# Kernel tuning notes

Measured on AMD Instinct MI355X. Metric: run time of the kernel, lower is better.

Reference implementation:

```python
import jax, jax.numpy as jnp
import numpy as np

N_HEADS = 16
THRESHOLD = 0.01
GROWTH_RATE = 0.05
NEG_INF = -1e30


def setup_inputs() -> dict:
    key = jax.random.key(0)
    k1, k2, k3, k4, k5 = jax.random.split(key, 5)
    B, T, C = 2, 2048, 1024
    s_in = 1.0 / np.sqrt(C)
    return {
        "x": jax.random.normal(k1, (B, T, C), dtype=jnp.float32),
        "Wqkv": jax.random.normal(k2, (C, 3 * C), dtype=jnp.float32) * s_in,
        "bqkv": jnp.zeros((3 * C,), dtype=jnp.float32),
        "Wout": jax.random.normal(k3, (C, C), dtype=jnp.float32) * s_in,
        "bout": jnp.zeros((C,), dtype=jnp.float32),
    }


def reference(x, Wqkv, bqkv, Wout, bout):
    B, T, C = x.shape
    H = N_HEADS
    D = C // H
    scale = jnp.float32(np.sqrt(D))

    qkv = x @ Wqkv + bqkv                         # [B,T,3C]
    qkv = qkv.reshape(B, T, 3, H, D)
    q = qkv[:, :, 0].transpose(0, 2, 1, 3)        # [B,H,T,D]
    k = qkv[:, :, 1].transpose(0, 2, 1, 3)
    v = qkv[:, :, 2].transpose(0, 2, 1, 3)

    scores = jnp.einsum('bhtd,bhsd->bhts', q, k) / scale   # [B,H,T,T]
    causal = jnp.tril(jnp.ones((T, T), dtype=bool))
    scores = jnp.where(causal, scores, NEG_INF)
    attn = jax.nn.softmax(scores, axis=-1)

    # neuroplastic sparsification: threshold prune + random regrow
    # (training-mode path; fixed key for determinism, dropout treated as identity/eval)
    regrow = jax.random.uniform(jax.random.key(42), attn.shape) < GROWTH_RATE
    keep = jnp.logical_or(attn > THRESHOLD, regrow)
    attn = attn * keep.astype(attn.dtype)

    out = jnp.einsum('bhts,bhsd->bhtd', attn, v)  # [B,H,T,D]
    out = out.transpose(0, 2, 1, 3).reshape(B, T, C)
    return out @ Wout + bout
```

## Files before the change

kernel.cpp:

```cpp
#include <hip/hip_runtime.h>
#include <stdint.h>


typedef _Float16 half8 __attribute__((ext_vector_type(8)));
typedef _Float16 half4 __attribute__((ext_vector_type(4)));
typedef float f32x4 __attribute__((ext_vector_type(4)));

#define MFMA16(a, b, c) __builtin_amdgcn_mfma_f32_16x16x32_f16(a, b, c, 0, 0, 0)

__device__ __forceinline__ void gld16(const void* g, void* l) {
  __builtin_amdgcn_global_load_lds(
      (const __attribute__((address_space(1))) void*)g,
      (__attribute__((address_space(3))) void*)l, 16, 0, 0);
}

__device__ __forceinline__ uint32_t rotl32(uint32_t x, uint32_t d) {
  return (x << d) | (x >> (32u - d));
}

__device__ __forceinline__ bool regrow(uint32_t b, uint32_t hts) {
  const uint32_t ks1 = 42u;
  const uint32_t ks2 = 0x1BD11BDAu ^ 42u;
  uint32_t x0 = 0u;
  uint32_t x1 = b * 0x4000000u + hts;
  x1 += ks1;
#define TF_R(r) { x0 += x1; x1 = rotl32(x1, r); x1 ^= x0; }
  TF_R(13) TF_R(15) TF_R(26) TF_R(6)  x0 += ks1; x1 += ks2 + 1u;
  TF_R(17) TF_R(29) TF_R(16) TF_R(24) x0 += ks2; x1 += 0u  + 2u;
  TF_R(13) TF_R(15) TF_R(26) TF_R(6)  x0 += 0u;  x1 += ks1 + 3u;
  TF_R(17) TF_R(29) TF_R(16) TF_R(24) x0 += ks1; x1 += ks2 + 4u;
  TF_R(13) TF_R(15) TF_R(26) TF_R(6)  x0 += ks2; x1 += 0u  + 5u;
#undef TF_R
  uint32_t r32 = x0 ^ x1;
  float f = __uint_as_float((r32 >> 9) | 0x3f800000u) - 1.0f;
  return f < 0.05f;
}

__global__ __launch_bounds__(256) void conv_x(const float* __restrict__ x,
                                              _Float16* __restrict__ xh,
                                              _Float16* __restrict__ xl) {
  int idx = blockIdx.x * 256 + threadIdx.x;
  int row = idx >> 7;
  int c8 = (idx & 127) << 3;
  const float* s = x + (size_t)row * 1024 + c8;
  float4 v0 = *(const float4*)s;
  float4 v1 = *(const float4*)(s + 4);
  float vv[8] = {v0.x, v0.y, v0.z, v0.w, v1.x, v1.y, v1.z, v1.w};
  half8 hh, ll;
#pragma unroll
  for (int i = 0; i < 8; ++i) {
    hh[i] = (_Float16)vv[i];
    ll[i] = (_Float16)(vv[i] - (float)hh[i]);
  }
  size_t o = (size_t)row * 1024 + (c8 ^ ((row & 7) << 3));
  *(half8*)&xh[o] = hh;
  *(half8*)&xl[o] = ll;
}

__global__ __launch_bounds__(256) void conv_w(const float* __restrict__ W, int N,
                                              _Float16* __restrict__ Wth,
                                              _Float16* __restrict__ Wtl) {
  __shared__ float sW[64][68];
  const int n0 = blockIdx.x * 64, k0 = blockIdx.y * 64;
  const int t = threadIdx.x;
  const int kr = t >> 2, nc = (t & 3) * 16;
#pragma unroll
  for (int j = 0; j < 4; ++j)
    *(float4*)&sW[kr][nc + 4 * j] =
        *(const float4*)&W[(size_t)(k0 + kr) * N + n0 + nc + 4 * j];
  __syncthreads();
  const int nl = t >> 2, ks = (t & 3) * 16;
#pragma unroll
  for (int j = 0; j < 2; ++j) {
    int k8 = ks + j * 8;
    half8 hh, ll;
#pragma unroll
    for (int e = 0; e < 8; ++e) {
      float v = sW[k8 + e][nl];
      hh[e] = (_Float16)v;
      ll[e] = (_Float16)(v - (float)hh[e]);
    }
    size_t o = (size_t)(n0 + nl) * 1024 + ((k0 + k8) ^ (((n0 + nl) & 7) << 3));
    *(half8*)&Wth[o] = hh;
    *(half8*)&Wtl[o] = ll;
  }
}

template <int PRE>
__global__ __launch_bounds__(256) void gemm_f16x3(
    const _Float16* __restrict__ Ah, const _Float16* __restrict__ Al,
    const float* __restrict__ Afp,
    const _Float16* __restrict__ Bth, const _Float16* __restrict__ Btl,
    const float* __restrict__ bias, int N, int outMode,
    _Float16* __restrict__ Qh, _Float16* __restrict__ Ql,
    _Float16* __restrict__ Kh, _Float16* __restrict__ Kl,
    _Float16* __restrict__ Vt, float* __restrict__ out)
{
  __shared__ _Float16 sAh[8192], sAl[8192], sBh[8192], sBl[8192];
  const int tid = threadIdx.x;
  const int wv = tid >> 6, lane = tid & 63;
  const int lg = lane >> 4, m15 = lane & 15;
  const int wr = wv >> 1, wc = wv & 1;
  const int m0 = blockIdx.y << 7, n0 = blockIdx.x << 7;
  const int srow = lane >> 3;
  const int schk = (lane & 7) << 3;

  f32x4 acc[4][4];
#pragma unroll
  for (int i = 0; i < 4; ++i)
#pragma unroll
    for (int j = 0; j < 4; ++j) acc[i][j] = (f32x4){0.f, 0.f, 0.f, 0.f};

  for (int g = 0; g < 16; ++g) {
    __syncthreads();
#pragma unroll
    for (int i = 0; i < 4; ++i) {
      int rb = (wv << 5) + (i << 3);
      size_t so = (size_t)(n0 + rb + srow) * 1024 + (g << 6) + schk;
      gld16(Bth + so, &sBh[rb << 6]);
      gld16(Btl + so, &sBl[rb << 6]);
    }
    if (PRE) {
#pragma unroll
      for (int i = 0; i < 4; ++i) {
        int rb = (wv << 5) + (i << 3);
        size_t so = (size_t)(m0 + rb + srow) * 1024 + (g << 6) + schk;
        gld16(Ah + so, &sAh[rb << 6]);
        gld16(Al + so, &sAl[rb << 6]);
      }
    } else {
      int r = tid >> 1, c0 = (tid & 1) << 5;
      const float* src = Afp + (size_t)(m0 + r) * 1024 + (g << 6) + c0;
#pragma unroll
      for (int i = 0; i < 8; ++i) {
        float4 v = *(const float4*)(src + (i << 2));
        half4 hh = {(_Float16)v.x, (_Float16)v.y, (_Float16)v.z, (_Float16)v.w};
        half4 ll = {(_Float16)(v.x - (float)hh[0]), (_Float16)(v.y - (float)hh[1]),
                    (_Float16)(v.z - (float)hh[2]), (_Float16)(v.w - (float)hh[3])};
        int off = (r << 6) + ((c0 + (i << 2)) ^ ((r & 7) << 3));
        *(half4*)&sAh[off] = hh;
        *(half4*)&sAl[off] = ll;
      }
    }
    __syncthreads();

#pragma unroll
    for (int ks = 0; ks < 2; ++ks) {
      half8 ah[4], al[4], bh[4], bl[4];
#pragma unroll
      for (int mi = 0; mi < 4; ++mi) {
        int row = (wr << 6) + (mi << 4) + m15;
        int off = (row << 6) + (((ks << 5) + (lg << 3)) ^ ((row & 7) << 3));
        ah[mi] = *(const half8*)&sAh[off];
        al[mi] = *(const half8*)&sAl[off];
      }
#pragma unroll
      for (int nj = 0; nj < 4; ++nj) {
        int row = (wc << 6) + (nj << 4) + m15;
        int off = (row << 6) + (((ks << 5) + (lg << 3)) ^ ((row & 7) << 3));
        bh[nj] = *(const half8*)&sBh[off];
        bl[nj] = *(const half8*)&sBl[off];
      }
#pragma unroll
      for (int mi = 0; mi < 4; ++mi)
#pragma unroll
        for (int nj = 0; nj < 4; ++nj) {
          acc[mi][nj] = MFMA16(ah[mi], bh[nj], acc[mi][nj]);
          acc[mi][nj] = MFMA16(ah[mi], bl[nj], acc[mi][nj]);
          acc[mi][nj] = MFMA16(al[mi], bh[nj], acc[mi][nj]);
        }
    }
  }

#pragma unroll
  for (int nj = 0; nj < 4; ++nj) {
    int n = n0 + (wc << 6) + (nj << 4) + m15;
    float bv = bias[n];
    int which = n >> 10;
    int hh_ = (n & 1023) >> 6;
    int d = n & 63;
#pragma unroll
    for (int mi = 0; mi < 4; ++mi) {
#pragma unroll
      for (int r = 0; r < 4; ++r) {
        int m = m0 + (wr << 6) + (mi << 4) + (lg << 2) + r;
        float v = acc[mi][nj][r] + bv;
        if (outMode == 1) {
          out[(size_t)m * N + n] = v;
        } else {
          _Float16 hi = (_Float16)v;
          _Float16 lo = (_Float16)(v - (float)hi);
          int b = m >> 11, t = m & 2047;
          if (which == 2) {
            size_t o = ((size_t)((b << 4) + hh_) * 64 + d) * 2048
                     + (t ^ ((d & 7) << 3));
            Vt[o] = hi;
          } else {
            size_t o = ((size_t)((b << 4) + hh_) * 2048 + t) * 64
                     + (d ^ ((t & 7) << 3));
            if (which == 0) { Qh[o] = hi; Ql[o] = lo; }
            else            { Kh[o] = hi; Kl[o] = lo; }
          }
        }
      }
    }
  }
}

__global__ __launch_bounds__(256) void attn_mfma(
    const _Float16* __restrict__ Qhg, const _Float16* __restrict__ Qlg,
    const _Float16* __restrict__ Khg, const _Float16* __restrict__ Klg,
    const _Float16* __restrict__ Vtg,
    _Float16* __restrict__ AOh, _Float16* __restrict__ AOl)
{
  __shared__ _Float16 sQh[4096], sQl[4096], sKh[4096], sKl[4096];
  __shared__ _Float16 sVt[4096], sP[4096];

  const int tid = threadIdx.x;
  const int wv = tid >> 6, lane = tid & 63;
  const int lg = lane >> 4, m15 = lane & 15;
  const int h = blockIdx.y, b = blockIdx.z;
  const size_t bh = (size_t)(b * 16 + h);
  const _Float16* Qhb = Qhg + bh * 2048 * 64;
  const _Float16* Qlb = Qlg + bh * 2048 * 64;
  const _Float16* Khb = Khg + bh * 2048 * 64;
  const _Float16* Klb = Klg + bh * 2048 * 64;
  const _Float16* Vtb = Vtg + bh * 64 * 2048;

  const int srow = lane >> 3, schk = (lane & 7) << 3;
  const int w16 = wv << 4;

  for (int hv = 0; hv < 2; ++hv) {
    const int qt = hv ? (31 - (int)blockIdx.x) : (int)blockIdx.x;
    const int t0 = qt << 6;

    __syncthreads();
    {
      size_t o0 = (size_t)(t0 + w16 + srow) * 64 + schk;
      size_t o1 = (size_t)(t0 + w16 + 8 + srow) * 64 + schk;
      gld16(Qhb + o0, &sQh[w16 << 6]);
      gld16(Qhb + o1, &sQh[(w16 + 8) << 6]);
      gld16(Qlb + o0, &sQl[w16 << 6]);
      gld16(Qlb + o1, &sQl[(w16 + 8) << 6]);
    }
    __syncthreads();

    const int qrow = w16 + m15;
    const int qsw = (qrow & 7) << 3;
    const half8 qh0 = *(const half8*)&sQh[(qrow << 6) + ((lg << 3) ^ qsw)];
    const half8 qh1 = *(const half8*)&sQh[(qrow << 6) + (((lg << 3) + 32) ^ qsw)];
    const half8 ql0 = *(const half8*)&sQl[(qrow << 6) + ((lg << 3) ^ qsw)];
    const half8 ql1 = *(const half8*)&sQl[(qrow << 6) + (((lg << 3) + 32) ^ qsw)];

    float m_[4], l_[4];
#pragma unroll
    for (int r = 0; r < 4; ++r) { m_[r] = -INFINITY; l_[r] = 0.0f; }

    for (int kt = 0; kt <= qt; ++kt) {
      __syncthreads();
      {
        size_t o0 = (size_t)((kt << 6) + w16 + srow) * 64 + schk;
        size_t o1 = (size_t)((kt << 6) + w16 + 8 + srow) * 64 + schk;
        gld16(Khb + o0, &sKh[w16 << 6]);
        gld16(Khb + o1, &sKh[(w16 + 8) << 6]);
        gld16(Klb + o0, &sKl[w16 << 6]);
        gld16(Klb + o1, &sKl[(w16 + 8) << 6]);
      }
      __syncthreads();

      float sc[4][4];
#pragma unroll
      for (int nt = 0; nt < 4; ++nt) {
        const int krow = (nt << 4) + m15;
        const int ksw = (krow & 7) << 3;
        half8 kh0 = *(const half8*)&sKh[(krow << 6) + ((lg << 3) ^ ksw)];
        half8 kh1 = *(const half8*)&sKh[(krow << 6) + (((lg << 3) + 32) ^ ksw)];
        half8 kl0 = *(const half8*)&sKl[(krow << 6) + ((lg << 3) ^ ksw)];
        half8 kl1 = *(const half8*)&sKl[(krow << 6) + (((lg << 3) + 32) ^ ksw)];
        f32x4 c = {0.f, 0.f, 0.f, 0.f};
        c = MFMA16(qh0, kh0, c);
        c = MFMA16(qh1, kh1, c);
        c = MFMA16(qh0, kl0, c);
        c = MFMA16(qh1, kl1, c);
        c = MFMA16(ql0, kh0, c);
        c = MFMA16(ql1, kh1, c);
#pragma unroll
        for (int r = 0; r < 4; ++r) {
          float s = c[r] * 0.125f;
          if (kt == qt && ((nt << 4) + m15) > (w16 + (lg << 2) + r)) s = -1e30f;
          sc[nt][r] = s;
        }
      }
#pragma unroll
      for (int r = 0; r < 4; ++r) {
        float tm = fmaxf(fmaxf(sc[0][r], sc[1][r]), fmaxf(sc[2][r], sc[3][r]));
        tm = fmaxf(tm, __shfl_xor(tm, 1));
        tm = fmaxf(tm, __shfl_xor(tm, 2));
        tm = fmaxf(tm, __shfl_xor(tm, 4));
        tm = fmaxf(tm, __shfl_xor(tm, 8));
        float mn = fmaxf(m_[r], tm);
        float ps = __expf(sc[0][r] - mn) + __expf(sc[1][r] - mn)
                 + __expf(sc[2][r] - mn) + __expf(sc[3][r] - mn);
        ps += __shfl_xor(ps, 1);
        ps += __shfl_xor(ps, 2);
        ps += __shfl_xor(ps, 4);
        ps += __shfl_xor(ps, 8);
        l_[r] = l_[r] * __expf(m_[r] - mn) + ps;
        m_[r] = mn;
      }
    }

    float rl[4];
#pragma unroll
    for (int r = 0; r < 4; ++r) rl[r] = 1.0f / l_[r];

    f32x4 oacc[4];
#pragma unroll
    for (int nt = 0; nt < 4; ++nt) oacc[nt] = (f32x4){0.f, 0.f, 0.f, 0.f};

    const uint32_t hqbase = (uint32_t)(h * 2048 + t0 + w16 + (lg << 2)) * 2048u;

    for (int kt = 0; kt <= qt; ++kt) {
      __syncthreads();
      {
        size_t o0 = (size_t)((kt << 6) + w16 + srow) * 64 + schk;
        size_t o1 = (size_t)((kt << 6) + w16 + 8 + srow) * 64 + schk;
        gld16(Khb + o0, &sKh[w16 << 6]);
        gld16(Khb + o1, &sKh[(w16 + 8) << 6]);
        gld16(Klb + o0, &sKl[w16 << 6]);
        gld16(Klb + o1, &sKl[(w16 + 8) << 6]);
        size_t v0 = (size_t)(w16 + srow) * 2048 + (kt << 6) + schk;
        size_t v1 = (size_t)(w16 + 8 + srow) * 2048 + (kt << 6) + schk;
        gld16(Vtb + v0, &sVt[w16 << 6]);
        gld16(Vtb + v1, &sVt[(w16 + 8) << 6]);
      }
      __syncthreads();

      float sc[4][4];
#pragma unroll
      for (int nt = 0; nt < 4; ++nt) {
        const int krow = (nt << 4) + m15;
        const int ksw = (krow & 7) << 3;
        half8 kh0 = *(const half8*)&sKh[(krow << 6) + ((lg << 3) ^ ksw)];
        half8 kh1 = *(const half8*)&sKh[(krow << 6) + (((lg << 3) + 32) ^ ksw)];
        half8 kl0 = *(const half8*)&sKl[(krow << 6) + ((lg << 3) ^ ksw)];
        half8 kl1 = *(const half8*)&sKl[(krow << 6) + (((lg << 3) + 32) ^ ksw)];
        f32x4 c = {0.f, 0.f, 0.f, 0.f};
        c = MFMA16(qh0, kh0, c);
        c = MFMA16(qh1, kh1, c);
        c = MFMA16(qh0, kl0, c);
        c = MFMA16(qh1, kl1, c);
        c = MFMA16(ql0, kh0, c);
        c = MFMA16(ql1, kh1, c);
#pragma unroll
        for (int r = 0; r < 4; ++r) {
          float s = c[r] * 0.125f;
          if (kt == qt && ((nt << 4) + m15) > (w16 + (lg << 2) + r)) s = -1e30f;
          sc[nt][r] = s;
        }
      }

#pragma unroll
      for (int nt = 0; nt < 4; ++nt) {
#pragma unroll
        for (int r = 0; r < 4; ++r) {
          float pv = __expf(sc[nt][r] - m_[r]) * rl[r];
          float outp = 0.0f;
          if (pv > 0.01f) {
            outp = pv;
          } else if (pv > 0.0f) {
            uint32_t hts = hqbase + (uint32_t)r * 2048u
                         + (uint32_t)((kt << 6) + (nt << 4) + m15);
            if (regrow((uint32_t)b, hts)) outp = pv;
          }
          int q = w16 + (lg << 2) + r;
          sP[(q << 6) + (((nt << 4) + m15) ^ ((q & 7) << 3))] = (_Float16)outp;
        }
      }
      __syncthreads();

      const int prow = w16 + m15;
      const int psw = (prow & 7) << 3;
      half8 pa0 = *(const half8*)&sP[(prow << 6) + ((lg << 3) ^ psw)];
      half8 pa1 = *(const half8*)&sP[(prow << 6) + (((lg << 3) + 32) ^ psw)];
#pragma unroll
      for (int nt = 0; nt < 4; ++nt) {
        const int vrow = (nt << 4) + m15;
        const int vsw = (vrow & 7) << 3;
        half8 vb0 = *(const half8*)&sVt[(vrow << 6) + ((lg << 3) ^ vsw)];
        half8 vb1 = *(const half8*)&sVt[(vrow << 6) + (((lg << 3) + 32) ^ vsw)];
        oacc[nt] = MFMA16(pa0, vb0, oacc[nt]);
        oacc[nt] = MFMA16(pa1, vb1, oacc[nt]);
      }
    }

#pragma unroll
    for (int nt = 0; nt < 4; ++nt)
#pragma unroll
      for (int r = 0; r < 4; ++r) {
        int q = t0 + w16 + (lg << 2) + r;
        int col = (h << 6) + (nt << 4) + m15;
        int mrow = (b << 11) + q;
        float v = oacc[nt][r];
        _Float16 hi = (_Float16)v;
        _Float16 lo = (_Float16)(v - (float)hi);
        size_t o = (size_t)mrow * 1024 + (col ^ ((mrow & 7) << 3));
        AOh[o] = hi;
        AOl[o] = lo;
      }
  }
}

extern "C" void kernel_launch(void* const* d_in, const int* in_sizes, int n_in,
                              void* d_out, int out_size, void* d_ws, size_t ws_size,
                              hipStream_t stream) {
  const float* x    = (const float*)d_in[0];
  const float* Wqkv = (const float*)d_in[1];
  const float* bqkv = (const float*)d_in[2];
  const float* Wout = (const float*)d_in[3];
  const float* bout = (const float*)d_in[4];
  float* out = (float*)d_out;

  const size_t MB = 1u << 20;
  char* w = (char*)d_ws;
  _Float16* Qh = (_Float16*)(w);
  _Float16* Ql = (_Float16*)(w + 8 * MB);
  _Float16* Kh = (_Float16*)(w + 16 * MB);
  _Float16* Kl = (_Float16*)(w + 24 * MB);
  _Float16* Vt = (_Float16*)(w + 32 * MB);

  const bool pre = (ws_size >= 72 * MB);
  _Float16 *xh, *xl, *Wqh, *Wql, *Woh, *Wol, *AOh, *AOl;
  if (pre) {
    xh  = (_Float16*)(w + 40 * MB);
    xl  = (_Float16*)(w + 48 * MB);
    Wqh = (_Float16*)(w + 56 * MB);
    Wql = (_Float16*)(w + 62 * MB);
    Woh = (_Float16*)(w + 68 * MB);
    Wol = (_Float16*)(w + 70 * MB);
  } else {
    xh = xl = nullptr;
    Wqh = (_Float16*)(w + 40 * MB);
    Wql = (_Float16*)(w + 46 * MB);
    Woh = (_Float16*)(w + 56 * MB);
    Wol = (_Float16*)(w + 58 * MB);
  }
  AOh = (_Float16*)(w + 40 * MB);
  AOl = (_Float16*)(w + 48 * MB);

  dim3 blk(256);
  if (pre) conv_x<<<2048, blk, 0, stream>>>(x, xh, xl);
  conv_w<<<dim3(48, 16), blk, 0, stream>>>(Wqkv, 3072, Wqh, Wql);
  conv_w<<<dim3(16, 16), blk, 0, stream>>>(Wout, 1024, Woh, Wol);

  if (pre)
    gemm_f16x3<1><<<dim3(24, 32), blk, 0, stream>>>(
        xh, xl, nullptr, Wqh, Wql, bqkv, 3072, 0, Qh, Ql, Kh, Kl, Vt, nullptr);
  else
    gemm_f16x3<0><<<dim3(24, 32), blk, 0, stream>>>(
        nullptr, nullptr, x, Wqh, Wql, bqkv, 3072, 0, Qh, Ql, Kh, Kl, Vt, nullptr);

  attn_mfma<<<dim3(16, 16, 2), blk, 0, stream>>>(Qh, Ql, Kh, Kl, Vt, AOh, AOl);

  gemm_f16x3<1><<<dim3(8, 32), blk, 0, stream>>>(
      AOh, AOl, nullptr, Woh, Wol, bout, 1024, 1,
      nullptr, nullptr, nullptr, nullptr, nullptr, out);
}
```

Before: 494.4 us.

## Use 128-row query tiles with 8 waves per attention block

The attention kernel now runs 512 threads per block, each block handling one 128-row query tile instead of two paired 64-row tiles. Each K/V tile loaded into shared memory is reused by twice as many query rows, halving per-query K/V traffic and barrier count. Blocks are ordered largest-first, but work per block is now imbalanced across the causal triangle rather than balanced by pairing. Shared memory per block grows and register pressure is capped by the larger launch bound.

Measured after the change: 699.9 us. 1.42x slower.

```diff
diff --git a/kernel.cpp b/kernel.cpp
--- a/kernel.cpp
+++ b/kernel.cpp
@@ -207,14 +207,16 @@
   }
 }
 
-__global__ __launch_bounds__(256) void attn_mfma(
+__global__ __launch_bounds__(512) void attn_mfma(
     const _Float16* __restrict__ Qhg, const _Float16* __restrict__ Qlg,
     const _Float16* __restrict__ Khg, const _Float16* __restrict__ Klg,
     const _Float16* __restrict__ Vtg,
     _Float16* __restrict__ AOh, _Float16* __restrict__ AOl)
 {
-  __shared__ _Float16 sQh[4096], sQl[4096], sKh[4096], sKl[4096];
-  __shared__ _Float16 sVt[4096], sP[4096];
+  __shared__ _Float16 sQh[8192], sQl[8192];
+  __shared__ _Float16 sKh[4096], sKl[4096];
+  __shared__ _Float16 sVt[4096];
+  __shared__ _Float16 sP[8192];
 
   const int tid = threadIdx.x;
   const int wv = tid >> 6, lane = tid & 63;
@@ -229,186 +231,181 @@
 
   const int srow = lane >> 3, schk = (lane & 7) << 3;
   const int w16 = wv << 4;
-
-  for (int hv = 0; hv < 2; ++hv) {
-    const int qt = hv ? (31 - (int)blockIdx.x) : (int)blockIdx.x;
-    const int t0 = qt << 6;
-
+  const int w8 = wv << 3;
+
+  const int qt = 15 - (int)blockIdx.x;
+  const int t0 = qt << 7;
+  const int ktmax = 2 * qt + 1;
+
+  {
+    size_t o0 = (size_t)(t0 + w16 + srow) * 64 + schk;
+    size_t o1 = (size_t)(t0 + w16 + 8 + srow) * 64 + schk;
+    gld16(Qhb + o0, &sQh[w16 << 6]);
+    gld16(Qhb + o1, &sQh[(w16 + 8) << 6]);
+    gld16(Qlb + o0, &sQl[w16 << 6]);
+    gld16(Qlb + o1, &sQl[(w16 + 8) << 6]);
+  }
+  __syncthreads();
+
+  const int qrow = w16 + m15;
+  const int qsw = (qrow & 7) << 3;
+  const half8 qh0 = *(const half8*)&sQh[(qrow << 6) + ((lg << 3) ^ qsw)];
+  const half8 qh1 = *(const half8*)&sQh[(qrow << 6) + (((lg << 3) + 32) ^ qsw)];
+  const half8 ql0 = *(const half8*)&sQl[(qrow << 6) + ((lg << 3) ^ qsw)];
+  const half8 ql1 = *(const half8*)&sQl[(qrow << 6) + (((lg << 3) + 32) ^ qsw)];
+
+  const int qg = t0 + w16 + (lg << 2);
+
+  float m_[4], l_[4];
+#pragma unroll
+  for (int r = 0; r < 4; ++r) { m_[r] = -INFINITY; l_[r] = 0.0f; }
+
+  for (int kt = 0; kt <= ktmax; ++kt) {
     __syncthreads();
     {
-      size_t o0 = (size_t)(t0 + w16 + srow) * 64 + schk;
-      size_t o1 = (size_t)(t0 + w16 + 8 + srow) * 64 + schk;
-      gld16(Qhb + o0, &sQh[w16 << 6]);
-      gld16(Qhb + o1, &sQh[(w16 + 8) << 6]);
-      gld16(Qlb + o0, &sQl[w16 << 6]);
-      gld16(Qlb + o1, &sQl[(w16 + 8) << 6]);
-    }
-    __syncthreads();
-
-    const int qrow = w16 + m15;
-    const int qsw = (qrow & 7) << 3;
-    const half8 qh0 = *(const half8*)&sQh[(qrow << 6) + ((lg << 3) ^ qsw)];
-    const half8 qh1 = *(const half8*)&sQh[(qrow << 6) + (((lg << 3) + 32) ^ qsw)];
-    const half8 ql0 = *(const half8*)&sQl[(qrow << 6) + ((lg << 3) ^ qsw)];
-    const half8 ql1 = *(const half8*)&sQl[(qrow << 6) + (((lg << 3) + 32) ^ qsw)];
-
-    float m_[4], l_[4];
-#pragma unroll
-    for (int r = 0; r < 4; ++r) { m_[r] = -INFINITY; l_[r] = 0.0f; }
-
-    for (int kt = 0; kt <= qt; ++kt) {
-      __syncthreads();
-      {
-        size_t o0 = (size_t)((kt << 6) + w16 + srow) * 64 + schk;
-        size_t o1 = (size_t)((kt << 6) + w16 + 8 + srow) * 64 + schk;
-        gld16(Khb + o0, &sKh[w16 << 6]);
-        gld16(Khb + o1, &sKh[(w16 + 8) << 6]);
-        gld16(Klb + o0, &sKl[w16 << 6]);
-        gld16(Klb + o1, &sKl[(w16 + 8) << 6]);
-      }
-      __syncthreads();
-
-      float sc[4][4];
-#pragma unroll
-      for (int nt = 0; nt < 4; ++nt) {
-        const int krow = (nt << 4) + m15;
-        const int ksw = (krow & 7) << 3;
-        half8 kh0 = *(const half8*)&sKh[(krow << 6) + ((lg << 3) ^ ksw)];
-        half8 kh1 = *(const half8*)&sKh[(krow << 6) + (((lg << 3) + 32) ^ ksw)];
-        half8 kl0 = *(const half8*)&sKl[(krow << 6) + ((lg << 3) ^ ksw)];
-        half8 kl1 = *(const half8*)&sKl[(krow << 6) + (((lg << 3) + 32) ^ ksw)];
-        f32x4 c = {0.f, 0.f, 0.f, 0.f};
-        c = MFMA16(qh0, kh0, c);
-        c = MFMA16(qh1, kh1, c);
-        c = MFMA16(qh0, kl0, c);
-        c = MFMA16(qh1, kl1, c);
-        c = MFMA16(ql0, kh0, c);
-        c = MFMA16(ql1, kh1, c);
-#pragma unroll
-        for (int r = 0; r < 4; ++r) {
-          float s = c[r] * 0.125f;
-          if (kt == qt && ((nt << 4) + m15) > (w16 + (lg << 2) + r)) s = -1e30f;
-          sc[nt][r] = s;
+      size_t o = (size_t)((kt << 6) + w8 + srow) * 64 + schk;
+      gld16(Khb + o, &sKh[w8 << 6]);
+      gld16(Klb + o, &sKl[w8 << 6]);
+    }
+    __syncthreads();
+
+    float sc[4][4];
+#pragma unroll
+    for (int nt = 0; nt < 4; ++nt) {
+      const int krow = (nt << 4) + m15;
+      const int ksw = (krow & 7) << 3;
+      half8 kh0 = *(const half8*)&sKh[(krow << 6) + ((lg << 3) ^ ksw)];
+      half8 kh1 = *(const half8*)&sKh[(krow << 6) + (((lg << 3) + 32) ^ ksw)];
+      half8 kl0 = *(const half8*)&sKl[(krow << 6) + ((lg << 3) ^ ksw)];
+      half8 kl1 = *(const half8*)&sKl[(krow << 6) + (((lg << 3) + 32) ^ ksw)];
+      f32x4 c = {0.f, 0.f, 0.f, 0.f};
+      c = MFMA16(qh0, kh0, c);
+      c = MFMA16(qh1, kh1, c);
+      c = MFMA16(qh0, kl0, c);
+      c = MFMA16(qh1, kl1, c);
+      c = MFMA16(ql0, kh0, c);
+      c = MFMA16(ql1, kh1, c);
+      const int sg = (kt << 6) + (nt << 4) + m15;
+#pragma unroll
+      for (int r = 0; r < 4; ++r) {
+        float s = c[r] * 0.125f;
+        if (kt >= 2 * qt && sg > qg + r) s = -1e30f;
+        sc[nt][r] = s;
+      }
+    }
+#pragma unroll
+    for (int r = 0; r < 4; ++r) {
+      float tm = fmaxf(fmaxf(sc[0][r], sc[1][r]), fmaxf(sc[2][r], sc[3][r]));
+      tm = fmaxf(tm, __shfl_xor(tm, 1));
+      tm = fmaxf(tm, __shfl_xor(tm, 2));
+      tm = fmaxf(tm, __shfl_xor(tm, 4));
+      tm = fmaxf(tm, __shfl_xor(tm, 8));
+      float mn = fmaxf(m_[r], tm);
+      float ps = __expf(sc[0][r] - mn) + __expf(sc[1][r] - mn)
+               + __expf(sc[2][r] - mn) + __expf(sc[3][r] - mn);
+      ps += __shfl_xor(ps, 1);
+      ps += __shfl_xor(ps, 2);
+      ps += __shfl_xor(ps, 4);
+      ps += __shfl_xor(ps, 8);
+      l_[r] = l_[r] * __expf(m_[r] - mn) + ps;
+      m_[r] = mn;
+    }
+  }
+
+  float rl[4];
+#pragma unroll
+  for (int r = 0; r < 4; ++r) rl[r] = 1.0f / l_[r];
+
+  f32x4 oacc[4];
+#pragma unroll
+  for (int nt = 0; nt < 4; ++nt) oacc[nt] = (f32x4){0.f, 0.f, 0.f, 0.f};
+
+  const uint32_t hqbase = (uint32_t)(h * 2048 + qg) * 2048u;
+
+  for (int kt = 0; kt <= ktmax; ++kt) {
+    __syncthreads();
+    {
+      size_t o = (size_t)((kt << 6) + w8 + srow) * 64 + schk;
+      gld16(Khb + o, &sKh[w8 << 6]);
+      gld16(Klb + o, &sKl[w8 << 6]);
+      size_t vo = (size_t)(w8 + srow) * 2048 + (kt << 6) + schk;
+      gld16(Vtb + vo, &sVt[w8 << 6]);
+    }
+    __syncthreads();
+
+    float sc[4][4];
+#pragma unroll
+    for (int nt = 0; nt < 4; ++nt) {
+      const int krow = (nt << 4) + m15;
+      const int ksw = (krow & 7) << 3;
+      half8 kh0 = *(const half8*)&sKh[(krow << 6) + ((lg << 3) ^ ksw)];
+      half8 kh1 = *(const half8*)&sKh[(krow << 6) + (((lg << 3) + 32) ^ ksw)];
+      half8 kl0 = *(const half8*)&sKl[(krow << 6) + ((lg << 3) ^ ksw)];
+      half8 kl1 = *(const half8*)&sKl[(krow << 6) + (((lg << 3) + 32) ^ ksw)];
+      f32x4 c = {0.f, 0.f, 0.f, 0.f};
+      c = MFMA16(qh0, kh0, c);
+      c = MFMA16(qh1, kh1, c);
+      c = MFMA16(qh0, kl0, c);
+      c = MFMA16(qh1, kl1, c);
+      c = MFMA16(ql0, kh0, c);
+      c = MFMA16(ql1, kh1, c);
+      const int sg = (kt << 6) + (nt << 4) + m15;
+#pragma unroll
+      for (int r = 0; r < 4; ++r) {
+        float s = c[r] * 0.125f;
+        if (kt >= 2 * qt && sg > qg + r) s = -1e30f;
+        sc[nt][r] = s;
+      }
+    }
+
+#pragma unroll
+    for (int nt = 0; nt < 4; ++nt) {
+#pragma unroll
+      for (int r = 0; r < 4; ++r) {
+        float pv = __expf(sc[nt][r] - m_[r]) * rl[r];
+        float outp = 0.0f;
+        if (pv > 0.01f) {
+          outp = pv;
+        } else if (pv > 0.0f) {
+          uint32_t hts = hqbase + (uint32_t)r * 2048u
+                       + (uint32_t)((kt << 6) + (nt << 4) + m15);
+          if (regrow((uint32_t)b, hts)) outp = pv;
         }
-      }
-#pragma unroll
-      for (int r = 0; r < 4; ++r) {
-        float tm = fmaxf(fmaxf(sc[0][r], sc[1][r]), fmaxf(sc[2][r], sc[3][r]));
-        tm = fmaxf(tm, __shfl_xor(tm, 1));
-        tm = fmaxf(tm, __shfl_xor(tm, 2));
-        tm = fmaxf(tm, __shfl_xor(tm, 4));
-        tm = fmaxf(tm, __shfl_xor(tm, 8));
-        float mn = fmaxf(m_[r], tm);
-        float ps = __expf(sc[0][r] - mn) + __expf(sc[1][r] - mn)
-                 + __expf(sc[2][r] - mn) + __expf(sc[3][r] - mn);
-        ps += __shfl_xor(ps, 1);
-        ps += __shfl_xor(ps, 2);
-        ps += __shfl_xor(ps, 4);
-        ps += __shfl_xor(ps, 8);
-        l_[r] = l_[r] * __expf(m_[r] - mn) + ps;
-        m_[r] = mn;
-      }
-    }
-
-    float rl[4];
-#pragma unroll
-    for (int r = 0; r < 4; ++r) rl[r] = 1.0f / l_[r];
-
-    f32x4 oacc[4];
-#pragma unroll
-    for (int nt = 0; nt < 4; ++nt) oacc[nt] = (f32x4){0.f, 0.f, 0.f, 0.f};
-
-    const uint32_t hqbase = (uint32_t)(h * 2048 + t0 + w16 + (lg << 2)) * 2048u;
-
-    for (int kt = 0; kt <= qt; ++kt) {
-      __syncthreads();
-      {
-        size_t o0 = (size_t)((kt << 6) + w16 + srow) * 64 + schk;
-        size_t o1 = (size_t)((kt << 6) + w16 + 8 + srow) * 64 + schk;
-        gld16(Khb + o0, &sKh[w16 << 6]);
-        gld16(Khb + o1, &sKh[(w16 + 8) << 6]);
-        gld16(Klb + o0, &sKl[w16 << 6]);
-        gld16(Klb + o1, &sKl[(w16 + 8) << 6]);
-        size_t v0 = (size_t)(w16 + srow) * 2048 + (kt << 6) + schk;
-        size_t v1 = (size_t)(w16 + 8 + srow) * 2048 + (kt << 6) + schk;
-        gld16(Vtb + v0, &sVt[w16 << 6]);
-        gld16(Vtb + v1, &sVt[(w16 + 8) << 6]);
-      }
-      __syncthreads();
-
-      float sc[4][4];
-#pragma unroll
-      for (int nt = 0; nt < 4; ++nt) {
-        const int krow = (nt << 4) + m15;
-        const int ksw = (krow & 7) << 3;
-        half8 kh0 = *(const half8*)&sKh[(krow << 6) + ((lg << 3) ^ ksw)];
-        half8 kh1 = *(const half8*)&sKh[(krow << 6) + (((lg << 3) + 32) ^ ksw)];
-        half8 kl0 = *(const half8*)&sKl[(krow << 6) + ((lg << 3) ^ ksw)];
-        half8 kl1 = *(const half8*)&sKl[(krow << 6) + (((lg << 3) + 32) ^ ksw)];
-        f32x4 c = {0.f, 0.f, 0.f, 0.f};
-        c = MFMA16(qh0, kh0, c);
-        c = MFMA16(qh1, kh1, c);
-        c = MFMA16(qh0, kl0, c);
-        c = MFMA16(qh1, kl1, c);
-        c = MFMA16(ql0, kh0, c);
-        c = MFMA16(ql1, kh1, c);
-#pragma unroll
-        for (int r = 0; r < 4; ++r) {
-          float s = c[r] * 0.125f;
-          if (kt == qt && ((nt << 4) + m15) > (w16 + (lg << 2) + r)) s = -1e30f;
-          sc[nt][r] = s;
-        }
-      }
-
-#pragma unroll
-      for (int nt = 0; nt < 4; ++nt) {
-#pragma unroll
-        for (int r = 0; r < 4; ++r) {
-          float pv = __expf(sc[nt][r] - m_[r]) * rl[r];
-          float outp = 0.0f;
-          if (pv > 0.01f) {
-            outp = pv;
-          } else if (pv > 0.0f) {
-            uint32_t hts = hqbase + (uint32_t)r * 2048u
-                         + (uint32_t)((kt << 6) + (nt << 4) + m15);
-            if (regrow((uint32_t)b, hts)) outp = pv;
-          }
-          int q = w16 + (lg << 2) + r;
-          sP[(q << 6) + (((nt << 4) + m15) ^ ((q & 7) << 3))] = (_Float16)outp;
-        }
-      }
-      __syncthreads();
-
-      const int prow = w16 + m15;
-      const int psw = (prow & 7) << 3;
-      half8 pa0 = *(const half8*)&sP[(prow << 6) + ((lg << 3) ^ psw)];
-      half8 pa1 = *(const half8*)&sP[(prow << 6) + (((lg << 3) + 32) ^ psw)];
-#pragma unroll
-      for (int nt = 0; nt < 4; ++nt) {
-        const int vrow = (nt << 4) + m15;
-        const int vsw = (vrow & 7) << 3;
-        half8 vb0 = *(const half8*)&sVt[(vrow << 6) + ((lg << 3) ^ vsw)];
-        half8 vb1 = *(const half8*)&sVt[(vrow << 6) + (((lg << 3) + 32) ^ vsw)];
-        oacc[nt] = MFMA16(pa0, vb0, oacc[nt]);
-        oacc[nt] = MFMA16(pa1, vb1, oacc[nt]);
-      }
-    }
-
-#pragma unroll
-    for (int nt = 0; nt < 4; ++nt)
-#pragma unroll
-      for (int r = 0; r < 4; ++r) {
-        int q = t0 + w16 + (lg << 2) + r;
-        int col = (h << 6) + (nt << 4) + m15;
-        int mrow = (b << 11) + q;
-        float v = oacc[nt][r];
-        _Float16 hi = (_Float16)v;
-        _Float16 lo = (_Float16)(v - (float)hi);
-        size_t o = (size_t)mrow * 1024 + (col ^ ((mrow & 7) << 3));
-        AOh[o] = hi;
-        AOl[o] = lo;
-      }
-  }
+        int q = w16 + (lg << 2) + r;
+        sP[(q << 6) + (((nt << 4) + m15) ^ ((q & 7) << 3))] = (_Float16)outp;
+      }
+    }
+    __syncthreads();
+
+    const int prow = w16 + m15;
+    const int psw = (prow & 7) << 3;
+    half8 pa0 = *(const half8*)&sP[(prow << 6) + ((lg << 3) ^ psw)];
+    half8 pa1 = *(const half8*)&sP[(prow << 6) + (((lg << 3) + 32) ^ psw)];
+#pragma unroll
+    for (int nt = 0; nt < 4; ++nt) {
+      const int vrow = (nt << 4) + m15;
+      const int vsw = (vrow & 7) << 3;
+      half8 vb0 = *(const half8*)&sVt[(vrow << 6) + ((lg << 3) ^ vsw)];
+      half8 vb1 = *(const half8*)&sVt[(vrow << 6) + (((lg << 3) + 32) ^ vsw)];
+      oacc[nt] = MFMA16(pa0, vb0, oacc[nt]);
+      oacc[nt] = MFMA16(pa1, vb1, oacc[nt]);
+    }
+  }
+
+#pragma unroll
+  for (int nt = 0; nt < 4; ++nt)
+#pragma unroll
+    for (int r = 0; r < 4; ++r) {
+      int q = qg + r;
+      int col = (h << 6) + (nt << 4) + m15;
+      int mrow = (b << 11) + q;
+      float v = oacc[nt][r];
+      _Float16 hi = (_Float16)v;
+      _Float16 lo = (_Float16)(v - (float)hi);
+      size_t o = (size_t)mrow * 1024 + (col ^ ((mrow & 7) << 3));
+      AOh[o] = hi;
+      AOl[o] = lo;
+    }
 }
 
 extern "C" void kernel_launch(void* const* d_in, const int* in_sizes, int n_in,
@@ -460,7 +457,8 @@
     gemm_f16x3<0><<<dim3(24, 32), blk, 0, stream>>>(
         nullptr, nullptr, x, Wqh, Wql, bqkv, 3072, 0, Qh, Ql, Kh, Kl, Vt, nullptr);
 
-  attn_mfma<<<dim3(16, 16, 2), blk, 0, stream>>>(Qh, Ql, Kh, Kl, Vt, AOh, AOl);
+  attn_mfma<<<dim3(16, 16, 2), dim3(512), 0, stream>>>(Qh, Ql, Kh, Kl, Vt,
+                                                       AOh, AOl);
 
   gemm_f16x3<1><<<dim3(8, 32), blk, 0, stream>>>(
       AOh, AOl, nullptr, Woh, Wol, bout, 1024, 1,
```

## Double-buffer K/V tiles in attention loops with split waitcnt and raw barriers

Applied to the files above, without the earlier changes.

Double-buffers the K (hi/lo) and V^T shared-memory tiles in both attention passes. The next tile's global-to-LDS loads are issued before computing on the current tile, and partial vmcnt waits let those loads overlap with the MFMA work. __syncthreads is replaced by raw s_barrier plus explicit waitcnt and sched_barrier fences. This hides global load latency behind compute, at the cost of more LDS per block (about 48KB to 72KB), which may lower occupancy.

After: 461.9 us. -6.6%, faster.

```diff
diff --git a/kernel.cpp b/kernel.cpp
--- a/kernel.cpp
+++ b/kernel.cpp
@@ -7,6 +7,8 @@
 typedef float f32x4 __attribute__((ext_vector_type(4)));
 
 #define MFMA16(a, b, c) __builtin_amdgcn_mfma_f32_16x16x32_f16(a, b, c, 0, 0, 0)
+#define SBAR() __builtin_amdgcn_s_barrier()
+#define SCHED0() __builtin_amdgcn_sched_barrier(0)
 
 __device__ __forceinline__ void gld16(const void* g, void* l) {
   __builtin_amdgcn_global_load_lds(
@@ -213,8 +215,10 @@
     const _Float16* __restrict__ Vtg,
     _Float16* __restrict__ AOh, _Float16* __restrict__ AOl)
 {
-  __shared__ _Float16 sQh[4096], sQl[4096], sKh[4096], sKl[4096];
-  __shared__ _Float16 sVt[4096], sP[4096];
+  __shared__ _Float16 sQh[4096], sQl[4096];
+  __shared__ _Float16 sKh[2][4096], sKl[2][4096];
+  __shared__ _Float16 sVt[2][4096];
+  __shared__ _Float16 sP[4096];
 
   const int tid = threadIdx.x;
   const int wv = tid >> 6, lane = tid & 63;
@@ -256,27 +260,43 @@
 #pragma unroll
     for (int r = 0; r < 4; ++r) { m_[r] = -INFINITY; l_[r] = 0.0f; }
 
+    {
+      size_t o0 = (size_t)(w16 + srow) * 64 + schk;
+      size_t o1 = (size_t)(w16 + 8 + srow) * 64 + schk;
+      gld16(Khb + o0, &sKh[0][w16 << 6]);
+      gld16(Khb + o1, &sKh[0][(w16 + 8) << 6]);
+      gld16(Klb + o0, &sKl[0][w16 << 6]);
+      gld16(Klb + o1, &sKl[0][(w16 + 8) << 6]);
+    }
+
     for (int kt = 0; kt <= qt; ++kt) {
-      __syncthreads();
-      {
-        size_t o0 = (size_t)((kt << 6) + w16 + srow) * 64 + schk;
-        size_t o1 = (size_t)((kt << 6) + w16 + 8 + srow) * 64 + schk;
-        gld16(Khb + o0, &sKh[w16 << 6]);
-        gld16(Khb + o1, &sKh[(w16 + 8) << 6]);
-        gld16(Klb + o0, &sKl[w16 << 6]);
-        gld16(Klb + o1, &sKl[(w16 + 8) << 6]);
-      }
-      __syncthreads();
+      const int cur = kt & 1;
+      SBAR();
+      SCHED0();
+      if (kt < qt) {
+        size_t o0 = (size_t)(((kt + 1) << 6) + w16 + srow) * 64 + schk;
+        size_t o1 = (size_t)(((kt + 1) << 6) + w16 + 8 + srow) * 64 + schk;
+        gld16(Khb + o0, &sKh[cur ^ 1][w16 << 6]);
+        gld16(Khb + o1, &sKh[cur ^ 1][(w16 + 8) << 6]);
+        gld16(Klb + o0, &sKl[cur ^ 1][w16 << 6]);
+        gld16(Klb + o1, &sKl[cur ^ 1][(w16 + 8) << 6]);
+        asm volatile("s_waitcnt vmcnt(4)" ::: "memory");
+      } else {
+        asm volatile("s_waitcnt vmcnt(0)" ::: "memory");
+      }
+      SCHED0();
+      SBAR();
+      SCHED0();
 
       float sc[4][4];
 #pragma unroll
       for (int nt = 0; nt < 4; ++nt) {
         const int krow = (nt << 4) + m15;
         const int ksw = (krow & 7) << 3;
-        half8 kh0 = *(const half8*)&sKh[(krow << 6) + ((lg << 3) ^ ksw)];
-        half8 kh1 = *(const half8*)&sKh[(krow << 6) + (((lg << 3) + 32) ^ ksw)];
-        half8 kl0 = *(const half8*)&sKl[(krow << 6) + ((lg << 3) ^ ksw)];
-        half8 kl1 = *(const half8*)&sKl[(krow << 6) + (((lg << 3) + 32) ^ ksw)];
+        half8 kh0 = *(const half8*)&sKh[cur][(krow << 6) + ((lg << 3) ^ ksw)];
+        half8 kh1 = *(const half8*)&sKh[cur][(krow << 6) + (((lg << 3) + 32) ^ ksw)];
+        half8 kl0 = *(const half8*)&sKl[cur][(krow << 6) + ((lg << 3) ^ ksw)];
+        half8 kl1 = *(const half8*)&sKl[cur][(krow << 6) + (((lg << 3) + 32) ^ ksw)];
         f32x4 c = {0.f, 0.f, 0.f, 0.f};
         c = MFMA16(qh0, kh0, c);
         c = MFMA16(qh1, kh1, c);
@@ -320,31 +340,53 @@
 
     const uint32_t hqbase = (uint32_t)(h * 2048 + t0 + w16 + (lg << 2)) * 2048u;
 
+    SBAR();
+    SCHED0();
+    {
+      size_t o0 = (size_t)(w16 + srow) * 64 + schk;
+      size_t o1 = (size_t)(w16 + 8 + srow) * 64 + schk;
+      gld16(Khb + o0, &sKh[0][w16 << 6]);
+      gld16(Khb + o1, &sKh[0][(w16 + 8) << 6]);
+      gld16(Klb + o0, &sKl[0][w16 << 6]);
+      gld16(Klb + o1, &sKl[0][(w16 + 8) << 6]);
+      size_t v0 = (size_t)(w16 + srow) * 2048 + schk;
+      size_t v1 = (size_t)(w16 + 8 + srow) * 2048 + schk;
+      gld16(Vtb + v0, &sVt[0][w16 << 6]);
+      gld16(Vtb + v1, &sVt[0][(w16 + 8) << 6]);
+    }
+
     for (int kt = 0; kt <= qt; ++kt) {
-      __syncthreads();
-      {
-        size_t o0 = (size_t)((kt << 6) + w16 + srow) * 64 + schk;
-        size_t o1 = (size_t)((kt << 6) + w16 + 8 + srow) * 64 + schk;
-        gld16(Khb + o0, &sKh[w16 << 6]);
-        gld16(Khb + o1, &sKh[(w16 + 8) << 6]);
-        gld16(Klb + o0, &sKl[w16 << 6]);
-        gld16(Klb + o1, &sKl[(w16 + 8) << 6]);
-        size_t v0 = (size_t)(w16 + srow) * 2048 + (kt << 6) + schk;
-        size_t v1 = (size_t)(w16 + 8 + srow) * 2048 + (kt << 6) + schk;
-        gld16(Vtb + v0, &sVt[w16 << 6]);
-        gld16(Vtb + v1, &sVt[(w16 + 8) << 6]);
-      }
-      __syncthreads();
+      const int cur = kt & 1;
+      SBAR();
+      SCHED0();
+      if (kt < qt) {
+        size_t o0 = (size_t)(((kt + 1) << 6) + w16 + srow) * 64 + schk;
+        size_t o1 = (size_t)(((kt + 1) << 6) + w16 + 8 + srow) * 64 + schk;
+        gld16(Khb + o0, &sKh[cur ^ 1][w16 << 6]);
+        gld16(Khb + o1, &sKh[cur ^ 1][(w16 + 8) << 6]);
+        gld16(Klb + o0, &sKl[cur ^ 1][w16 << 6]);
+        gld16(Klb + o1, &sKl[cur ^ 1][(w16 + 8) << 6]);
+        size_t v0 = (size_t)(w16 + srow) * 2048 + ((kt + 1) << 6) + schk;
+        size_t v1 = (size_t)(w16 + 8 + srow) * 2048 + ((kt + 1) << 6) + schk;
+        gld16(Vtb + v0, &sVt[cur ^ 1][w16 << 6]);
+        gld16(Vtb + v1, &sVt[cur ^ 1][(w16 + 8) << 6]);
+        asm volatile("s_waitcnt vmcnt(6)" ::: "memory");
+      } else {
+        asm volatile("s_waitcnt vmcnt(0)" ::: "memory");
+      }
+      SCHED0();
+      SBAR();
+      SCHED0();
 
       float sc[4][4];
 #pragma unroll
       for (int nt = 0; nt < 4; ++nt) {
         const int krow = (nt << 4) + m15;
         const int ksw = (krow & 7) << 3;
-        half8 kh0 = *(const half8*)&sKh[(krow << 6) + ((lg << 3) ^ ksw)];
-        half8 kh1 = *(const half8*)&sKh[(krow << 6) + (((lg << 3) + 32) ^ ksw)];
-        half8 kl0 = *(const half8*)&sKl[(krow << 6) + ((lg << 3) ^ ksw)];
-        half8 kl1 = *(const half8*)&sKl[(krow << 6) + (((lg << 3) + 32) ^ ksw)];
+        half8 kh0 = *(const half8*)&sKh[cur][(krow << 6) + ((lg << 3) ^ ksw)];
+        half8 kh1 = *(const half8*)&sKh[cur][(krow << 6) + (((lg << 3) + 32) ^ ksw)];
+        half8 kl0 = *(const half8*)&sKl[cur][(krow << 6) + ((lg << 3) ^ ksw)];
+        half8 kl1 = *(const half8*)&sKl[cur][(krow << 6) + (((lg << 3) + 32) ^ ksw)];
         f32x4 c = {0.f, 0.f, 0.f, 0.f};
         c = MFMA16(qh0, kh0, c);
         c = MFMA16(qh1, kh1, c);
@@ -377,7 +419,10 @@
           sP[(q << 6) + (((nt << 4) + m15) ^ ((q & 7) << 3))] = (_Float16)outp;
         }
       }
-      __syncthreads();
+      asm volatile("s_waitcnt lgkmcnt(0)" ::: "memory");
+      SCHED0();
+      SBAR();
+      SCHED0();
 
       const int prow = w16 + m15;
       const int psw = (prow & 7) << 3;
@@ -387,8 +432,8 @@
       for (int nt = 0; nt < 4; ++nt) {
         const int vrow = (nt << 4) + m15;
         const int vsw = (vrow & 7) << 3;
-        half8 vb0 = *(const half8*)&sVt[(vrow << 6) + ((lg << 3) ^ vsw)];
-        half8 vb1 = *(const half8*)&sVt[(vrow << 6) + (((lg << 3) + 32) ^ vsw)];
+        half8 vb0 = *(const half8*)&sVt[cur][(vrow << 6) + ((lg << 3) ^ vsw)];
+        half8 vb1 = *(const half8*)&sVt[cur][(vrow << 6) + (((lg << 3) + 32) ^ vsw)];
         oacc[nt] = MFMA16(pa0, vb0, oacc[nt]);
         oacc[nt] = MFMA16(pa1, vb1, oacc[nt]);
       }
```
